# Optimization experiments

Measured on AMD Instinct MI355X. Metric: run time of the kernel, lower is better.

The kernel has to match this reference:

```python
import jax, jax.numpy as jnp
import numpy as np

EPS = 1e-7  # K.epsilon()
ROUTINGS = 3


def squash(v, axis=-1):
    s2 = jnp.sum(jnp.square(v), axis=axis, keepdims=True)
    scale = s2 / (1.0 + s2) / jnp.sqrt(s2 + EPS)
    return scale * v


def setup_inputs() -> dict:
    key = jax.random.key(0)
    k1, k2 = jax.random.split(key)
    B, Ni, Di, No, Do = 64, 2048, 16, 32, 16
    inputs = jax.random.normal(k1, (B, Ni, Di), dtype=jnp.float32)
    # glorot-uniform-ish scale for W
    limit = np.sqrt(6.0 / (Di + Do)).astype(np.float32)
    W = jax.random.uniform(k2, (1, Ni, No, Do, Di), dtype=jnp.float32,
                           minval=-limit, maxval=limit)
    return {"inputs": inputs, "W": W}


def reference(inputs, W):
    # inputs: [B, Ni, Di]; W: [1, Ni, No, Do, Di]
    # inputs_hat[b,n,o,d] = sum_i W[n,o,d,i] * inputs[b,n,i]  -> [B, Ni, No, Do]
    inputs_hat = jnp.einsum('bni,nodi->bnod', inputs, W[0])
    B, Ni, No, _ = inputs_hat.shape
    b = jnp.zeros((B, Ni, No), dtype=inputs_hat.dtype)
    outputs = None
    for i in range(ROUTINGS):
        c = jax.nn.softmax(b, axis=2)              # [B, Ni, No]
        s = jnp.einsum('bnod,bno->bod', inputs_hat, c)  # weighted sum over Ni
        outputs = squash(s)                        # [B, No, Do]
        if i < ROUTINGS - 1:
            # NOTE: faithful to source — update uses sum over Do of c-weighted
            # inputs_hat (does NOT use `outputs`).
            b = b + jnp.sum(inputs_hat * c[..., None], axis=-1)
    return outputs
```

## Files before the change

kernel.cpp:

```cpp
#include <hip/hip_runtime.h>
#include <cmath>


#define NI 2048

typedef short bf16x8 __attribute__((ext_vector_type(8)));
typedef float f32x4 __attribute__((ext_vector_type(4)));

static __device__ __forceinline__ unsigned short f2bf(float f) {
  unsigned u = __float_as_uint(f);
  u += 0x7FFFu + ((u >> 16) & 1u);
  return (unsigned short)(u >> 16);
}
static __device__ __forceinline__ float bf2f(unsigned short h) {
  return __uint_as_float(((unsigned)h) << 16);
}
static __device__ __forceinline__ void split4(float4 v, uint2& hi, uint2& lo) {
  unsigned short h0 = f2bf(v.x), h1 = f2bf(v.y), h2 = f2bf(v.z), h3 = f2bf(v.w);
  unsigned short l0 = f2bf(v.x - bf2f(h0)), l1 = f2bf(v.y - bf2f(h1));
  unsigned short l2 = f2bf(v.z - bf2f(h2)), l3 = f2bf(v.w - bf2f(h3));
  hi.x = (unsigned)h0 | ((unsigned)h1 << 16); hi.y = (unsigned)h2 | ((unsigned)h3 << 16);
  lo.x = (unsigned)l0 | ((unsigned)l1 << 16); lo.y = (unsigned)l2 | ((unsigned)l3 << 16);
}

__global__ __launch_bounds__(256) void caps_c2_kernel(
    const float* __restrict__ x, const float* __restrict__ W,
    float* __restrict__ c2g)
{
  const int n = blockIdx.x;
  const int t = threadIdx.x;
  const int wv = t >> 6, l = t & 63;
  __shared__ __align__(16) float WdS[32 * 20];
  __shared__ float xs[64 * 17];
  __shared__ float c2s[64 * 33];

  {
    const int d = l >> 2, i4 = l & 3;
    #pragma unroll
    for (int m = 0; m < 8; ++m) {
      const int o = m * 4 + wv;
      float4 v = *(const float4*)(W + (size_t)n * 8192 + o * 256 + d * 16 + i4 * 4);
      float s0 = v.x, s1 = v.y, s2 = v.z, s3 = v.w;
      #pragma unroll
      for (int mk = 4; mk <= 32; mk <<= 1) {
        s0 += __shfl_xor(s0, mk); s1 += __shfl_xor(s1, mk);
        s2 += __shfl_xor(s2, mk); s3 += __shfl_xor(s3, mk);
      }
      if (l < 4) *(float4*)&WdS[o * 20 + l * 4] = make_float4(s0, s1, s2, s3);
    }
  }
  {
    const int i = t & 15;
    #pragma unroll
    for (int m = 0; m < 4; ++m) {
      int b = m * 16 + (t >> 4);
      xs[b * 17 + i] = x[(size_t)b * (NI * 16) + n * 16 + i];
    }
  }
  __syncthreads();

  {
    const int b = t >> 2, oq = t & 3;
    float h[8];
    #pragma unroll
    for (int jj = 0; jj < 8; ++jj) {
      const int o = oq + 4 * jj;
      float acc = 0.f;
      #pragma unroll
      for (int i = 0; i < 16; ++i) acc += WdS[o * 20 + i] * xs[b * 17 + i];
      h[jj] = acc;
    }
    float b1[8], e[8];
    float mx = -1e30f;
    #pragma unroll
    for (int jj = 0; jj < 8; ++jj) { b1[jj] = h[jj] * 0.03125f; mx = fmaxf(mx, b1[jj]); }
    mx = fmaxf(mx, __shfl_xor(mx, 1)); mx = fmaxf(mx, __shfl_xor(mx, 2));
    float S = 0.f;
    #pragma unroll
    for (int jj = 0; jj < 8; ++jj) { e[jj] = __expf(b1[jj] - mx); S += e[jj]; }
    S += __shfl_xor(S, 1); S += __shfl_xor(S, 2);
    float inv = 1.0f / S;
    float b2[8]; float mx2 = -1e30f;
    #pragma unroll
    for (int jj = 0; jj < 8; ++jj) { b2[jj] = b1[jj] + e[jj] * inv * h[jj]; mx2 = fmaxf(mx2, b2[jj]); }
    mx2 = fmaxf(mx2, __shfl_xor(mx2, 1)); mx2 = fmaxf(mx2, __shfl_xor(mx2, 2));
    float S2 = 0.f;
    #pragma unroll
    for (int jj = 0; jj < 8; ++jj) { e[jj] = __expf(b2[jj] - mx2); S2 += e[jj]; }
    S2 += __shfl_xor(S2, 1); S2 += __shfl_xor(S2, 2);
    float inv2 = 1.0f / S2;
    #pragma unroll
    for (int jj = 0; jj < 8; ++jj) c2s[b * 33 + oq + 4 * jj] = e[jj] * inv2;
  }
  __syncthreads();
  #pragma unroll
  for (int m = 0; m < 8; ++m) {
    int flat = m * 256 + t;
    c2g[(size_t)n * 2048 + flat] = c2s[(flat & 63) * 33 + (flat >> 6)];
  }
}

#define WAOFF 0
#define XBOFF 6144
#define C2OFF 7680
__global__ __launch_bounds__(512, 4) void caps_main_kernel(
    const float* __restrict__ x, const float* __restrict__ W,
    const float* __restrict__ c2, float* __restrict__ partial)
{
  const int bx = blockIdx.x;
  const int ng = bx >> 1, hh = bx & 1;
  const int t = threadIdx.x;
  const int wv = t >> 6, l = t & 63;
  const int q = l >> 4, dq = l & 15, qh = q & 1, s_a = q >> 1;
  const int bt = wv & 3, oct = wv >> 2;

  __shared__ __align__(16) float lds[8704];
  float* WA  = lds + WAOFF;
  float* XB  = lds + XBOFF;
  float* C2L = lds + C2OFF;

  float sacc[8][4];
  #pragma unroll
  for (int oo = 0; oo < 8; ++oo)
    { sacc[oo][0] = 0.f; sacc[oo][1] = 0.f; sacc[oo][2] = 0.f; sacc[oo][3] = 0.f; }

  const int n0 = ng * 8;
  const int wo = t >> 6;
  const int wd = (t >> 2) & 15, wi4 = t & 3;
  const int xb = t >> 3, xi = (t & 7) * 2;

  float4 wreg0 = *(const float4*)(W + (size_t)n0 * 8192 + hh * 4096 + 4 * t);
  float4 wreg1 = *(const float4*)(W + (size_t)n0 * 8192 + hh * 4096 + 4 * (t + 512));
  float2 xreg  = *(const float2*)(x + (size_t)xb * (NI * 16) + n0 * 16 + xi);
  float2 creg  = *(const float2*)(c2 + (size_t)n0 * 2048 + hh * 1024 + 2 * t);

  #pragma unroll 1
  for (int nn = 0; nn < 8; ++nn) {
    {
      uint2 hi, lo;
      split4(wreg0, hi, lo);
      int row = (wo * 32 + wd) * 12;
      *(uint2*)((char*)&WA[row] + wi4 * 8) = hi;
      *(uint2*)((char*)&WA[row + 16 * 12] + wi4 * 8) = lo;
      split4(wreg1, hi, lo);
      row = ((wo + 8) * 32 + wd) * 12;
      *(uint2*)((char*)&WA[row] + wi4 * 8) = hi;
      *(uint2*)((char*)&WA[row + 16 * 12] + wi4 * 8) = lo;
      unsigned short h0 = f2bf(xreg.x), h1 = f2bf(xreg.y);
      unsigned short g0 = f2bf(xreg.x - bf2f(h0)), g1 = f2bf(xreg.y - bf2f(h1));
      ((unsigned*)&XB[xb * 12])[xi >> 1]            = (unsigned)h0 | ((unsigned)h1 << 16);
      ((unsigned*)&XB[(64 + xb) * 12])[xi >> 1]     = (unsigned)g0 | ((unsigned)g1 << 16);
      *(float2*)&C2L[2 * t] = creg;
    }
    __syncthreads();

    if (nn < 7) {
      const size_t nb = (size_t)(n0 + nn + 1);
      wreg0 = *(const float4*)(W + nb * 8192 + hh * 4096 + 4 * t);
      wreg1 = *(const float4*)(W + nb * 8192 + hh * 4096 + 4 * (t + 512));
      xreg  = *(const float2*)(x + (size_t)xb * (NI * 16) + nb * 16 + xi);
      creg  = *(const float2*)(c2 + nb * 2048 + hh * 1024 + 2 * t);
    }

    bf16x8 B0 = *(const bf16x8*)&XB[(bt * 16 + dq) * 12 + qh * 4];
    bf16x8 B1 = *(const bf16x8*)&XB[(64 + bt * 16 + dq) * 12 + qh * 4];
    #pragma unroll
    for (int oo = 0; oo < 8; ++oo) {
      const int o = oct * 8 + oo;
      bf16x8 A = *(const bf16x8*)&WA[(o * 32 + s_a * 16 + dq) * 12 + qh * 4];
      f32x4 D = {0.f, 0.f, 0.f, 0.f};
      D = __builtin_amdgcn_mfma_f32_16x16x32_bf16(A, B0, D, 0, 0, 0);
      D = __builtin_amdgcn_mfma_f32_16x16x32_bf16(A, B1, D, 0, 0, 0);
      float c = C2L[o * 64 + bt * 16 + dq];
      sacc[oo][0] += c * D[0]; sacc[oo][1] += c * D[1];
      sacc[oo][2] += c * D[2]; sacc[oo][3] += c * D[3];
    }
    __syncthreads();
  }

  #pragma unroll
  for (int oo = 0; oo < 8; ++oo) {
    const int o = oct * 8 + oo;
    *(float4*)(partial + (size_t)ng * 32768 + (size_t)(bt * 16 + dq) * 512
               + (hh * 16 + o) * 16 + q * 4)
        = make_float4(sacc[oo][0], sacc[oo][1], sacc[oo][2], sacc[oo][3]);
  }
}

__global__ __launch_bounds__(256) void caps_reduce_kernel(
    const float* __restrict__ partial, float* __restrict__ out)
{
  const int t = threadIdx.x;
  const int w4 = t >> 6, ln = t & 63;
  const int pair = blockIdx.x * 4 + w4;
  const int b = pair >> 5, o = pair & 31;
  const int d = ln & 15, cg = ln >> 4;
  const float* p = partial + (size_t)b * 512 + o * 16 + d;
  float s = 0.f;
  #pragma unroll 8
  for (int gg = cg; gg < 256; gg += 4) s += p[(size_t)gg * 32768];
  s += __shfl_xor(s, 16); s += __shfl_xor(s, 32);
  float s2 = s * s;
  s2 += __shfl_xor(s2, 1); s2 += __shfl_xor(s2, 2);
  s2 += __shfl_xor(s2, 4); s2 += __shfl_xor(s2, 8);
  float scale = s2 / (1.0f + s2) / sqrtf(s2 + 1e-7f);
  if (ln < 16) out[(size_t)b * 512 + o * 16 + d] = scale * s;
}

extern "C" void kernel_launch(void* const* d_in, const int* in_sizes, int n_in,
                              void* d_out, int out_size, void* d_ws, size_t ws_size,
                              hipStream_t stream) {
  const float* x = (const float*)d_in[0];
  const float* W = (const float*)d_in[1];
  if (in_sizes[0] != 64 * 2048 * 16) { const float* tmp = x; x = W; W = tmp; }
  float* out = (float*)d_out;

  float* partial = (float*)d_ws;
  float* c2g     = partial + (size_t)256 * 32768;

  caps_c2_kernel<<<2048, 256, 0, stream>>>(x, W, c2g);
  caps_main_kernel<<<512, 512, 0, stream>>>(x, W, c2g, partial);
  caps_reduce_kernel<<<512, 256, 0, stream>>>(partial, out);
}
```

Measured before the change: 134.7 us.

## Fuse routing-coefficient computation into main MFMA kernel, split by batch half

New measurement: 126.7 us. -5.9%, faster.

```diff
diff --git a/kernel.cpp b/kernel.cpp
--- a/kernel.cpp
+++ b/kernel.cpp
@@ -23,101 +23,29 @@
   lo.x = (unsigned)l0 | ((unsigned)l1 << 16); lo.y = (unsigned)l2 | ((unsigned)l3 << 16);
 }
 
-__global__ __launch_bounds__(256) void caps_c2_kernel(
+#define WAOFF 0
+#define XBOFF 12288
+#define HOFF  13056
+#define C2OFF 14112
+#define LDSZ  15168
+__global__ __launch_bounds__(512, 4) void caps_fused_kernel(
     const float* __restrict__ x, const float* __restrict__ W,
-    float* __restrict__ c2g)
-{
-  const int n = blockIdx.x;
-  const int t = threadIdx.x;
-  const int wv = t >> 6, l = t & 63;
-  __shared__ __align__(16) float WdS[32 * 20];
-  __shared__ float xs[64 * 17];
-  __shared__ float c2s[64 * 33];
-
-  {
-    const int d = l >> 2, i4 = l & 3;
-    #pragma unroll
-    for (int m = 0; m < 8; ++m) {
-      const int o = m * 4 + wv;
-      float4 v = *(const float4*)(W + (size_t)n * 8192 + o * 256 + d * 16 + i4 * 4);
-      float s0 = v.x, s1 = v.y, s2 = v.z, s3 = v.w;
-      #pragma unroll
-      for (int mk = 4; mk <= 32; mk <<= 1) {
-        s0 += __shfl_xor(s0, mk); s1 += __shfl_xor(s1, mk);
-        s2 += __shfl_xor(s2, mk); s3 += __shfl_xor(s3, mk);
-      }
-      if (l < 4) *(float4*)&WdS[o * 20 + l * 4] = make_float4(s0, s1, s2, s3);
-    }
-  }
-  {
-    const int i = t & 15;
-    #pragma unroll
-    for (int m = 0; m < 4; ++m) {
-      int b = m * 16 + (t >> 4);
-      xs[b * 17 + i] = x[(size_t)b * (NI * 16) + n * 16 + i];
-    }
-  }
-  __syncthreads();
-
-  {
-    const int b = t >> 2, oq = t & 3;
-    float h[8];
-    #pragma unroll
-    for (int jj = 0; jj < 8; ++jj) {
-      const int o = oq + 4 * jj;
-      float acc = 0.f;
-      #pragma unroll
-      for (int i = 0; i < 16; ++i) acc += WdS[o * 20 + i] * xs[b * 17 + i];
-      h[jj] = acc;
-    }
-    float b1[8], e[8];
-    float mx = -1e30f;
-    #pragma unroll
-    for (int jj = 0; jj < 8; ++jj) { b1[jj] = h[jj] * 0.03125f; mx = fmaxf(mx, b1[jj]); }
-    mx = fmaxf(mx, __shfl_xor(mx, 1)); mx = fmaxf(mx, __shfl_xor(mx, 2));
-    float S = 0.f;
-    #pragma unroll
-    for (int jj = 0; jj < 8; ++jj) { e[jj] = __expf(b1[jj] - mx); S += e[jj]; }
-    S += __shfl_xor(S, 1); S += __shfl_xor(S, 2);
-    float inv = 1.0f / S;
-    float b2[8]; float mx2 = -1e30f;
-    #pragma unroll
-    for (int jj = 0; jj < 8; ++jj) { b2[jj] = b1[jj] + e[jj] * inv * h[jj]; mx2 = fmaxf(mx2, b2[jj]); }
-    mx2 = fmaxf(mx2, __shfl_xor(mx2, 1)); mx2 = fmaxf(mx2, __shfl_xor(mx2, 2));
-    float S2 = 0.f;
-    #pragma unroll
-    for (int jj = 0; jj < 8; ++jj) { e[jj] = __expf(b2[jj] - mx2); S2 += e[jj]; }
-    S2 += __shfl_xor(S2, 1); S2 += __shfl_xor(S2, 2);
-    float inv2 = 1.0f / S2;
-    #pragma unroll
-    for (int jj = 0; jj < 8; ++jj) c2s[b * 33 + oq + 4 * jj] = e[jj] * inv2;
-  }
-  __syncthreads();
-  #pragma unroll
-  for (int m = 0; m < 8; ++m) {
-    int flat = m * 256 + t;
-    c2g[(size_t)n * 2048 + flat] = c2s[(flat & 63) * 33 + (flat >> 6)];
-  }
-}
-
-#define WAOFF 0
-#define XBOFF 6144
-#define C2OFF 7680
-__global__ __launch_bounds__(512, 4) void caps_main_kernel(
-    const float* __restrict__ x, const float* __restrict__ W,
-    const float* __restrict__ c2, float* __restrict__ partial)
+    float* __restrict__ partial)
 {
   const int bx = blockIdx.x;
-  const int ng = bx >> 1, hh = bx & 1;
+  const int xcd = bx & 7, slot = bx >> 3;
+  const int ng = xcd * 32 + (slot >> 1);
+  const int bh = slot & 1;
   const int t = threadIdx.x;
   const int wv = t >> 6, l = t & 63;
   const int q = l >> 4, dq = l & 15, qh = q & 1, s_a = q >> 1;
-  const int bt = wv & 3, oct = wv >> 2;
+  const int bt = wv & 1, oq = wv >> 1;
 
-  __shared__ __align__(16) float lds[8704];
+  __shared__ __align__(16) float lds[LDSZ];
   float* WA  = lds + WAOFF;
   float* XB  = lds + XBOFF;
-  float* C2L = lds + C2OFF;
+  float* hS  = lds + HOFF;
+  float* c2S = lds + C2OFF;
 
   float sacc[8][4];
   #pragma unroll
@@ -125,64 +53,106 @@
     { sacc[oo][0] = 0.f; sacc[oo][1] = 0.f; sacc[oo][2] = 0.f; sacc[oo][3] = 0.f; }
 
   const int n0 = ng * 8;
-  const int wo = t >> 6;
-  const int wd = (t >> 2) & 15, wi4 = t & 3;
-  const int xb = t >> 3, xi = (t & 7) * 2;
+  const int wo0 = t >> 6, wd = (t >> 2) & 15, wi4 = t & 3;
+  const int xb = t >> 2, xi4 = t & 3;
 
-  float4 wreg0 = *(const float4*)(W + (size_t)n0 * 8192 + hh * 4096 + 4 * t);
-  float4 wreg1 = *(const float4*)(W + (size_t)n0 * 8192 + hh * 4096 + 4 * (t + 512));
-  float2 xreg  = *(const float2*)(x + (size_t)xb * (NI * 16) + n0 * 16 + xi);
-  float2 creg  = *(const float2*)(c2 + (size_t)n0 * 2048 + hh * 1024 + 2 * t);
+  float4 wreg[4];
+  #pragma unroll
+  for (int c = 0; c < 4; ++c)
+    wreg[c] = *(const float4*)(W + (size_t)n0 * 8192 + c * 2048 + 4 * t);
+  float4 xreg = make_float4(0.f, 0.f, 0.f, 0.f);
+  if (t < 128)
+    xreg = *(const float4*)(x + (size_t)(bh * 32 + xb) * (NI * 16) + n0 * 16 + xi4 * 4);
 
   #pragma unroll 1
   for (int nn = 0; nn < 8; ++nn) {
-    {
+    #pragma unroll
+    for (int c = 0; c < 4; ++c) {
       uint2 hi, lo;
-      split4(wreg0, hi, lo);
-      int row = (wo * 32 + wd) * 12;
+      split4(wreg[c], hi, lo);
+      const int row = ((c * 8 + wo0) * 32 + wd) * 12;
       *(uint2*)((char*)&WA[row] + wi4 * 8) = hi;
-      *(uint2*)((char*)&WA[row + 16 * 12] + wi4 * 8) = lo;
-      split4(wreg1, hi, lo);
-      row = ((wo + 8) * 32 + wd) * 12;
-      *(uint2*)((char*)&WA[row] + wi4 * 8) = hi;
-      *(uint2*)((char*)&WA[row + 16 * 12] + wi4 * 8) = lo;
-      unsigned short h0 = f2bf(xreg.x), h1 = f2bf(xreg.y);
-      unsigned short g0 = f2bf(xreg.x - bf2f(h0)), g1 = f2bf(xreg.y - bf2f(h1));
-      ((unsigned*)&XB[xb * 12])[xi >> 1]            = (unsigned)h0 | ((unsigned)h1 << 16);
-      ((unsigned*)&XB[(64 + xb) * 12])[xi >> 1]     = (unsigned)g0 | ((unsigned)g1 << 16);
-      *(float2*)&C2L[2 * t] = creg;
+      *(uint2*)((char*)&WA[row + 192] + wi4 * 8) = lo;
+    }
+    if (t < 128) {
+      uint2 hi, lo;
+      split4(xreg, hi, lo);
+      *(uint2*)((char*)&XB[xb * 12] + xi4 * 8) = hi;
+      *(uint2*)((char*)&XB[(32 + xb) * 12] + xi4 * 8) = lo;
     }
     __syncthreads();
 
     if (nn < 7) {
       const size_t nb = (size_t)(n0 + nn + 1);
-      wreg0 = *(const float4*)(W + nb * 8192 + hh * 4096 + 4 * t);
-      wreg1 = *(const float4*)(W + nb * 8192 + hh * 4096 + 4 * (t + 512));
-      xreg  = *(const float2*)(x + (size_t)xb * (NI * 16) + nb * 16 + xi);
-      creg  = *(const float2*)(c2 + nb * 2048 + hh * 1024 + 2 * t);
+      #pragma unroll
+      for (int c = 0; c < 4; ++c)
+        wreg[c] = *(const float4*)(W + nb * 8192 + c * 2048 + 4 * t);
+      if (t < 128)
+        xreg = *(const float4*)(x + (size_t)(bh * 32 + xb) * (NI * 16) + nb * 16 + xi4 * 4);
     }
 
-    bf16x8 B0 = *(const bf16x8*)&XB[(bt * 16 + dq) * 12 + qh * 4];
-    bf16x8 B1 = *(const bf16x8*)&XB[(64 + bt * 16 + dq) * 12 + qh * 4];
+    f32x4 Dv[8];
+    {
+      bf16x8 B0 = *(const bf16x8*)&XB[(bt * 16 + dq) * 12 + qh * 4];
+      bf16x8 B1 = *(const bf16x8*)&XB[(32 + bt * 16 + dq) * 12 + qh * 4];
+      #pragma unroll
+      for (int oo = 0; oo < 8; ++oo) {
+        const int o = oq * 8 + oo;
+        bf16x8 A = *(const bf16x8*)&WA[(o * 32 + s_a * 16 + dq) * 12 + qh * 4];
+        f32x4 D = {0.f, 0.f, 0.f, 0.f};
+        D = __builtin_amdgcn_mfma_f32_16x16x32_bf16(A, B0, D, 0, 0, 0);
+        D = __builtin_amdgcn_mfma_f32_16x16x32_bf16(A, B1, D, 0, 0, 0);
+        Dv[oo] = D;
+        float hs = D[0] + D[1] + D[2] + D[3];
+        hs += __shfl_xor(hs, 16);
+        hs += __shfl_xor(hs, 32);
+        if (q == 0) hS[(bt * 16 + dq) * 33 + o] = hs;
+      }
+    }
+    __syncthreads();
+
+    {
+      const int bl = t >> 4, op = t & 15;
+      const float h0 = hS[bl * 33 + op];
+      const float h1 = hS[bl * 33 + op + 16];
+      const float b10 = h0 * 0.03125f, b11 = h1 * 0.03125f;
+      float mx = fmaxf(b10, b11);
+      mx = fmaxf(mx, __shfl_xor(mx, 1)); mx = fmaxf(mx, __shfl_xor(mx, 2));
+      mx = fmaxf(mx, __shfl_xor(mx, 4)); mx = fmaxf(mx, __shfl_xor(mx, 8));
+      const float e0 = __expf(b10 - mx), e1 = __expf(b11 - mx);
+      float S = e0 + e1;
+      S += __shfl_xor(S, 1); S += __shfl_xor(S, 2);
+      S += __shfl_xor(S, 4); S += __shfl_xor(S, 8);
+      const float inv = 1.0f / S;
+      const float b20 = b10 + e0 * inv * h0, b21 = b11 + e1 * inv * h1;
+      float mx2 = fmaxf(b20, b21);
+      mx2 = fmaxf(mx2, __shfl_xor(mx2, 1)); mx2 = fmaxf(mx2, __shfl_xor(mx2, 2));
+      mx2 = fmaxf(mx2, __shfl_xor(mx2, 4)); mx2 = fmaxf(mx2, __shfl_xor(mx2, 8));
+      const float e20 = __expf(b20 - mx2), e21 = __expf(b21 - mx2);
+      float S2 = e20 + e21;
+      S2 += __shfl_xor(S2, 1); S2 += __shfl_xor(S2, 2);
+      S2 += __shfl_xor(S2, 4); S2 += __shfl_xor(S2, 8);
+      const float inv2 = 1.0f / S2;
+      c2S[op * 33 + bl] = e20 * inv2;
+      c2S[(op + 16) * 33 + bl] = e21 * inv2;
+    }
+    __syncthreads();
+
     #pragma unroll
     for (int oo = 0; oo < 8; ++oo) {
-      const int o = oct * 8 + oo;
-      bf16x8 A = *(const bf16x8*)&WA[(o * 32 + s_a * 16 + dq) * 12 + qh * 4];
-      f32x4 D = {0.f, 0.f, 0.f, 0.f};
-      D = __builtin_amdgcn_mfma_f32_16x16x32_bf16(A, B0, D, 0, 0, 0);
-      D = __builtin_amdgcn_mfma_f32_16x16x32_bf16(A, B1, D, 0, 0, 0);
-      float c = C2L[o * 64 + bt * 16 + dq];
-      sacc[oo][0] += c * D[0]; sacc[oo][1] += c * D[1];
-      sacc[oo][2] += c * D[2]; sacc[oo][3] += c * D[3];
+      const int o = oq * 8 + oo;
+      const float c = c2S[o * 33 + bt * 16 + dq];
+      sacc[oo][0] += c * Dv[oo][0]; sacc[oo][1] += c * Dv[oo][1];
+      sacc[oo][2] += c * Dv[oo][2]; sacc[oo][3] += c * Dv[oo][3];
     }
-    __syncthreads();
   }
 
+  float* pb = partial + (size_t)ng * 32768
+            + (size_t)(bh * 32 + bt * 16 + dq) * 512 + q * 4;
   #pragma unroll
   for (int oo = 0; oo < 8; ++oo) {
-    const int o = oct * 8 + oo;
-    *(float4*)(partial + (size_t)ng * 32768 + (size_t)(bt * 16 + dq) * 512
-               + (hh * 16 + o) * 16 + q * 4)
+    const int o = oq * 8 + oo;
+    *(float4*)(pb + o * 16)
         = make_float4(sacc[oo][0], sacc[oo][1], sacc[oo][2], sacc[oo][3]);
   }
 }
@@ -216,9 +186,7 @@
   float* out = (float*)d_out;
 
   float* partial = (float*)d_ws;
-  float* c2g     = partial + (size_t)256 * 32768;
 
-  caps_c2_kernel<<<2048, 256, 0, stream>>>(x, W, c2g);
-  caps_main_kernel<<<512, 512, 0, stream>>>(x, W, c2g, partial);
+  caps_fused_kernel<<<512, 512, 0, stream>>>(x, W, partial);
   caps_reduce_kernel<<<512, 256, 0, stream>>>(partial, out);
 }
```
